# Performance work log

Hardware: AMD Instinct MI355X
Metric: run time of the kernel (lower is better)

## Reference

```python
import jax, jax.numpy as jnp
import numpy as np

B, D_MODEL, H = 2048, 1024, 16
D_K = D_MODEL // H


def setup_inputs() -> dict:
    root = jax.random.key(0)
    ks = jax.random.split(root, 11)
    w_scale = 1.0 / np.sqrt(D_MODEL).astype(np.float32)
    inp = {
        "query": jax.random.normal(ks[0], (B, D_MODEL), jnp.float32),
        "key": jax.random.normal(ks[1], (B, D_MODEL), jnp.float32),
        "value": jax.random.normal(ks[2], (B, D_MODEL), jnp.float32),
        # Linear weights (used as x @ W + b)
        "Wq": jax.random.normal(ks[3], (D_MODEL, D_MODEL), jnp.float32) * w_scale,
        "bq": jnp.zeros((D_MODEL,), jnp.float32),
        "Wk": jax.random.normal(ks[4], (D_MODEL, D_MODEL), jnp.float32) * w_scale,
        "bk": jnp.zeros((D_MODEL,), jnp.float32),
        "Wv": jax.random.normal(ks[5], (D_MODEL, D_MODEL), jnp.float32) * w_scale,
        "bv": jnp.zeros((D_MODEL,), jnp.float32),
        # Random U drawn fresh each forward in torch; materialized here for determinism.
        # torch shape: randn(d_model, nbatches*d_k).view(nbatches, h, d_k, d_k)
        "U": jax.random.normal(ks[6], (B, H, D_K, D_K), jnp.float32),
    }
    return inp


def reference(query, key, value, Wq, bq, Wk, bk, Wv, bv, U):
    b, dm = query.shape
    h = U.shape[1]
    dk = dm // h
    residual = key
    # QKV projections, then view(b, -1, h, dk).transpose(1, 2) -> [b, h, 1, dk]
    q = (query @ Wq + bq).reshape(b, 1, h, dk).transpose(0, 2, 1, 3)
    k = (key @ Wk + bk).reshape(b, 1, h, dk).transpose(0, 2, 1, 3)
    v = (value @ Wv + bv).reshape(b, 1, h, dk).transpose(0, 2, 1, 3)
    # attn_weight = (q @ U) @ k^T : [b,h,1,dk] @ [b,h,dk,dk] @ [b,h,dk,1] -> [b,h,1,1]
    aw = jnp.matmul(q, U)
    scores = jnp.matmul(aw, jnp.swapaxes(k, -1, -2))
    p = jax.nn.softmax(scores, axis=-1)  # dropout is identity at inference
    # context = p^T @ v : [b,h,1,1] @ [b,h,1,dk] -> [b,h,1,dk]
    ctx = jnp.matmul(jnp.swapaxes(p, -1, -2), v)
    ctx = jnp.swapaxes(ctx, 1, 2).reshape(b, dm)
    return ctx + residual
```

## Files before the change

### kernel.cpp

```cpp
#include <hip/hip_runtime.h>
#include <hip/hip_bf16.h>


#define M_DIM 2048
#define N_DIM 1024
#define K_DIM 1024

typedef __attribute__((ext_vector_type(8))) short short8;
typedef __attribute__((ext_vector_type(4))) float f32x4;

__device__ inline unsigned rne_bf16(float f) {
    unsigned u = __builtin_bit_cast(unsigned, f);
    return (u + 0x7FFFu + ((u >> 16) & 1u)) >> 16;
}
__device__ inline unsigned pack2(float lo, float hi) {
    return rne_bf16(lo) | (rne_bf16(hi) << 16);
}

__global__ __launch_bounds__(256)
void convert_kernel(const float* __restrict__ value, const float* __restrict__ Wv,
                    short* __restrict__ Vb, short* __restrict__ WvTb) {
    __shared__ unsigned tr[64 * 33];
    const int b = blockIdx.x, tid = threadIdx.x;
    if (b < 1024) {
        int g = b * 256 + tid;
        int row = g >> 7, ch = g & 127;
        int kt = ch >> 3, c = ch & 7;
        int tm = row >> 6, r = row & 63;
        const float* p = value + (size_t)row * K_DIM + ch * 8;
        f32x4 a0 = *(const f32x4*)p;
        f32x4 a1 = *(const f32x4*)(p + 4);
        union { short8 s; unsigned u[4]; } o;
        o.u[0] = pack2(a0[0], a0[1]);
        o.u[1] = pack2(a0[2], a0[3]);
        o.u[2] = pack2(a1[0], a1[1]);
        o.u[3] = pack2(a1[2], a1[3]);
        *(short8*)&Vb[(size_t)(tm * 16 + kt) * 4096 + r * 64 + ((c ^ (r & 7)) << 3)] = o.s;
    } else {
        int b2 = b - 1024;
        int tn = b2 & 15, kt = b2 >> 4;
        #pragma unroll
        for (int s = 0; s < 2; ++s) {
            int kp = (tid >> 4) + s * 16;
            int n4 = (tid & 15) * 4;
            const float* bp = Wv + (size_t)(kt * 64 + 2 * kp) * N_DIM + tn * 64 + n4;
            f32x4 b0 = *(const f32x4*)bp;
            f32x4 b1 = *(const f32x4*)(bp + N_DIM);
            #pragma unroll
            for (int m = 0; m < 4; ++m)
                tr[(n4 + m) * 33 + kp] = pack2(b0[m], b1[m]);
        }
        __syncthreads();
        int n = tid >> 2;
        #pragma unroll
        for (int h = 0; h < 2; ++h) {
            int c = (tid & 3) + 4 * h;
            union { short8 s; unsigned u[4]; } o;
            #pragma unroll
            for (int p = 0; p < 4; ++p)
                o.u[p] = tr[n * 33 + c * 4 + p];
            *(short8*)&WvTb[(size_t)(tn * 16 + kt) * 4096 + n * 64 + ((c ^ (n & 7)) << 3)] = o.s;
        }
    }
}

__device__ inline void gl_lds16(const short* g, short* l) {
    __builtin_amdgcn_global_load_lds((const __attribute__((address_space(1))) void*)g,
                                     (__attribute__((address_space(3))) void*)l,
                                     16, 0, 0);
}

__global__ __launch_bounds__(256)
void gemm_kernel(const short* __restrict__ Vb, const short* __restrict__ WvTb,
                 const float* __restrict__ key, const float* __restrict__ bv,
                 float* __restrict__ out) {
    __shared__ __align__(16) short As[2][4096];
    __shared__ __align__(16) short Bs[2][4096];

    const int tid = threadIdx.x;
    const int bn = blockIdx.x;
    const int bm = blockIdx.y;
    const int lane = tid & 63;
    const int wid = tid >> 6;
    const int wr = wid >> 1;
    const int wc = wid & 1;

    const short* Abase = Vb + (size_t)bm * 16 * 4096;
    const short* Bbase = WvTb + (size_t)bn * 16 * 4096;

    f32x4 acc[2][2] = {};

    auto stage = [&](int buf, int kt) {
        const short* ga = Abase + (size_t)kt * 4096 + tid * 8;
        const short* gb = Bbase + (size_t)kt * 4096 + tid * 8;
        gl_lds16(ga,        &As[buf][tid * 8]);
        gl_lds16(ga + 2048, &As[buf][2048 + tid * 8]);
        gl_lds16(gb,        &Bs[buf][tid * 8]);
        gl_lds16(gb + 2048, &Bs[buf][2048 + tid * 8]);
    };

    auto compute = [&](int buf) {
        #pragma unroll
        for (int ks = 0; ks < 2; ++ks) {
            short8 afr[2], bfr[2];
            const int g = ks * 4 + (lane >> 4);
            #pragma unroll
            for (int fm = 0; fm < 2; ++fm) {
                int r = wr * 32 + fm * 16 + (lane & 15);
                afr[fm] = *(const short8*)&As[buf][r * 64 + ((g ^ (r & 7)) << 3)];
            }
            #pragma unroll
            for (int fn = 0; fn < 2; ++fn) {
                int n = wc * 32 + fn * 16 + (lane & 15);
                bfr[fn] = *(const short8*)&Bs[buf][n * 64 + ((g ^ (n & 7)) << 3)];
            }
            #pragma unroll
            for (int fm = 0; fm < 2; ++fm)
                #pragma unroll
                for (int fn = 0; fn < 2; ++fn)
                    acc[fm][fn] = __builtin_amdgcn_mfma_f32_16x16x32_bf16(
                        afr[fm], bfr[fn], acc[fm][fn], 0, 0, 0);
        }
    };

    stage(0, 0);
    __syncthreads();
    #pragma unroll 1
    for (int kt = 0; kt < 16; ++kt) {
        if (kt < 15) stage((kt + 1) & 1, kt + 1);
        compute(kt & 1);
        __syncthreads();
    }

    const int row0 = bm * 64, col0 = bn * 64;
    #pragma unroll
    for (int fm = 0; fm < 2; ++fm) {
        #pragma unroll
        for (int fn = 0; fn < 2; ++fn) {
            int col = col0 + wc * 32 + fn * 16 + (lane & 15);
            int rbase = row0 + wr * 32 + fm * 16 + ((lane >> 4) * 4);
            float b = bv[col];
            #pragma unroll
            for (int i = 0; i < 4; ++i) {
                int r = rbase + i;
                out[(size_t)r * N_DIM + col] = acc[fm][fn][i] + b + key[(size_t)r * N_DIM + col];
            }
        }
    }
}

extern "C" void kernel_launch(void* const* d_in, const int* in_sizes, int n_in,
                              void* d_out, int out_size, void* d_ws, size_t ws_size,
                              hipStream_t stream) {
    const float* key   = (const float*)d_in[1];
    const float* value = (const float*)d_in[2];
    const float* Wv    = (const float*)d_in[7];
    const float* bv    = (const float*)d_in[8];
    float* out = (float*)d_out;

    short* Vb   = (short*)d_ws;
    short* WvTb = (short*)d_ws + (size_t)M_DIM * N_DIM;

    convert_kernel<<<1024 + 256, 256, 0, stream>>>(value, Wv, Vb, WvTb);
    gemm_kernel<<<dim3(N_DIM / 64, M_DIM / 64), 256, 0, stream>>>(Vb, WvTb, key, bv, out);
}
```

Measured before the change: 23.42 us.

## Triple-buffer GEMM K-loop, swizzle block order, and prefetch epilogue operands

Measured after the change: 24.79 us. +5.8%, slower.

```diff
diff --git a/kernel.cpp b/kernel.cpp
--- a/kernel.cpp
+++ b/kernel.cpp
@@ -20,7 +20,7 @@
 __global__ __launch_bounds__(256)
 void convert_kernel(const float* __restrict__ value, const float* __restrict__ Wv,
                     short* __restrict__ Vb, short* __restrict__ WvTb) {
-    __shared__ unsigned tr[64 * 33];
+    __shared__ unsigned tr[64 * 36];
     const int b = blockIdx.x, tid = threadIdx.x;
     if (b < 1024) {
         int g = b * 256 + tid;
@@ -48,7 +48,7 @@
             f32x4 b1 = *(const f32x4*)(bp + N_DIM);
             #pragma unroll
             for (int m = 0; m < 4; ++m)
-                tr[(n4 + m) * 33 + kp] = pack2(b0[m], b1[m]);
+                tr[(n4 + m) * 36 + kp] = pack2(b0[m], b1[m]);
         }
         __syncthreads();
         int n = tid >> 2;
@@ -58,7 +58,7 @@
             union { short8 s; unsigned u[4]; } o;
             #pragma unroll
             for (int p = 0; p < 4; ++p)
-                o.u[p] = tr[n * 33 + c * 4 + p];
+                o.u[p] = tr[n * 36 + c * 4 + p];
             *(short8*)&WvTb[(size_t)(tn * 16 + kt) * 4096 + n * 64 + ((c ^ (n & 7)) << 3)] = o.s;
         }
     }
@@ -74,12 +74,14 @@
 void gemm_kernel(const short* __restrict__ Vb, const short* __restrict__ WvTb,
                  const float* __restrict__ key, const float* __restrict__ bv,
                  float* __restrict__ out) {
-    __shared__ __align__(16) short As[2][4096];
-    __shared__ __align__(16) short Bs[2][4096];
+    __shared__ __align__(16) short As[3][4096];
+    __shared__ __align__(16) short Bs[3][4096];
 
     const int tid = threadIdx.x;
-    const int bn = blockIdx.x;
-    const int bm = blockIdx.y;
+    const int bid = blockIdx.x;
+    const int swz = ((bid & 7) << 6) | (bid >> 3);
+    const int bm = swz >> 4;
+    const int bn = swz & 15;
     const int lane = tid & 63;
     const int wid = tid >> 6;
     const int wr = wid >> 1;
@@ -87,6 +89,21 @@
 
     const short* Abase = Vb + (size_t)bm * 16 * 4096;
     const short* Bbase = WvTb + (size_t)bn * 16 * 4096;
+    const int row0 = bm * 64, col0 = bn * 64;
+
+    const int colA = col0 + wc * 32 + (lane & 15);
+    const int rbaseA = row0 + wr * 32 + ((lane >> 4) * 4);
+    float keyr[2][2][4];
+    float bvr[2];
+    #pragma unroll
+    for (int fn = 0; fn < 2; ++fn) bvr[fn] = bv[colA + fn * 16];
+    #pragma unroll
+    for (int fm = 0; fm < 2; ++fm)
+        #pragma unroll
+        for (int fn = 0; fn < 2; ++fn)
+            #pragma unroll
+            for (int i = 0; i < 4; ++i)
+                keyr[fm][fn][i] = key[(size_t)(rbaseA + fm * 16 + i) * N_DIM + colA + fn * 16];
 
     f32x4 acc[2][2] = {};
 
@@ -124,26 +141,28 @@
     };
 
     stage(0, 0);
-    __syncthreads();
+    stage(1, 1);
+
     #pragma unroll 1
-    for (int kt = 0; kt < 16; ++kt) {
-        if (kt < 15) stage((kt + 1) & 1, kt + 1);
-        compute(kt & 1);
-        __syncthreads();
+    for (int kt = 0; kt < 15; ++kt) {
+        asm volatile("s_waitcnt vmcnt(4)" ::: "memory");
+        __builtin_amdgcn_s_barrier();
+        if (kt < 14) stage((kt + 2) % 3, kt + 2);
+        compute(kt % 3);
     }
+    asm volatile("s_waitcnt vmcnt(0)" ::: "memory");
+    __builtin_amdgcn_s_barrier();
+    compute(0);
 
-    const int row0 = bm * 64, col0 = bn * 64;
     #pragma unroll
     for (int fm = 0; fm < 2; ++fm) {
         #pragma unroll
         for (int fn = 0; fn < 2; ++fn) {
-            int col = col0 + wc * 32 + fn * 16 + (lane & 15);
-            int rbase = row0 + wr * 32 + fm * 16 + ((lane >> 4) * 4);
-            float b = bv[col];
+            int col = colA + fn * 16;
             #pragma unroll
             for (int i = 0; i < 4; ++i) {
-                int r = rbase + i;
-                out[(size_t)r * N_DIM + col] = acc[fm][fn][i] + b + key[(size_t)r * N_DIM + col];
+                int r = rbaseA + fm * 16 + i;
+                out[(size_t)r * N_DIM + col] = acc[fm][fn][i] + bvr[fn] + keyr[fm][fn][i];
             }
         }
     }
@@ -159,8 +178,8 @@
     float* out = (float*)d_out;
 
     short* Vb   = (short*)d_ws;
-    short* WvTb = (short*)d_ws + (size_t)M_DIM * N_DIM;
+    short* WvTb = (short*)d_ws + (size_t)M_DIM * K_DIM;
 
     convert_kernel<<<1024 + 256, 256, 0, stream>>>(value, Wv, Vb, WvTb);
-    gemm_kernel<<<dim3(N_DIM / 64, M_DIM / 64), 256, 0, stream>>>(Vb, WvTb, key, bv, out);
+    gemm_kernel<<<512, 256, 0, stream>>>(Vb, WvTb, key, bv, out);
 }
```
